# Kernel optimization log

Hardware: AMD Instinct MI355X
Metric: run time of the kernel (lower is better)

## Reference

```python
import jax, jax.numpy as jnp
import numpy as np

# Config matching init_kwargs: layer_nb=1 -> stride 16, image 608x608 -> 38x38 grid
B, CIN, H, W = 32, 512, 38, 38
NA, NC = 3, 80
STRIDE = 16.0
ANCHORS = np.array([[30.0, 61.0], [62.0, 45.0], [59.0, 119.0]], dtype=np.float32)


def setup_inputs() -> dict:
    key = jax.random.key(0)
    k1, k2, k3 = jax.random.split(key, 3)
    xin = jax.random.normal(k1, (B, CIN, H, W), dtype=jnp.float32)
    # 1x1 conv weight stored as (out_ch, in_ch); out_ch = NA*(NC+5) = 255
    conv_w = jax.random.normal(k2, (NA * (NC + 5), CIN), dtype=jnp.float32) * 0.02
    conv_b = jax.random.normal(k3, (NA * (NC + 5),), dtype=jnp.float32) * 0.01
    return {"xin": xin, "conv_w": conv_w, "conv_b": conv_b}


def reference(xin, conv_w, conv_b):
    # 1x1 conv == channel GEMM; fuse the NCHW->NHWC permute into the einsum
    fm = jnp.einsum('bchw,oc->bhwo', xin, conv_w) + conv_b  # [B,H,W,255]
    fm = fm.reshape(B, H, W, NA, NC + 5)
    tx, ty, tw, th = fm[..., 0], fm[..., 1], fm[..., 2], fm[..., 3]
    # grid offsets (precomputed via broadcasting instead of per-call numpy rebuild)
    x_off = jnp.arange(W, dtype=fm.dtype)[None, None, :, None]   # broadcast over B,H,NA
    y_off = jnp.arange(H, dtype=fm.dtype)[None, :, None, None]   # broadcast over B,W,NA
    anchors = jnp.asarray(ANCHORS, dtype=fm.dtype)               # [NA,2]
    bx = (jax.nn.sigmoid(tx) + x_off) * STRIDE
    by = (jax.nn.sigmoid(ty) + y_off) * STRIDE
    bw = jnp.exp(tw) * anchors[:, 0]
    bh = jnp.exp(th) * anchors[:, 1]
    boxes = jnp.stack([bx, by, bw, bh], axis=-1)                 # [B,H,W,NA,4]
    # concat decoded boxes with raw objectness + class logits -> [B,H,W,NA,85]
    return jnp.concatenate([boxes, fm[..., 4:]], axis=-1)
```

## Files before the change

kernel.cpp:

```cpp
#include <hip/hip_runtime.h>
#include <cstdint>
#include <cstddef>

#define CIN_K  512
#define WW_    38
#define BHW    1444
#define NOUT   255
#define MTOT   46208

#define BM 64
#define BK 32
#define KITERS (CIN_K / BK)
#define LDB 40
#define EPS_ 272

typedef __attribute__((ext_vector_type(8))) short  bf16x8;
typedef __attribute__((ext_vector_type(4))) float  floatx4;

static __device__ __forceinline__ unsigned f2bf(float f) {
    unsigned u = __builtin_bit_cast(unsigned, f);
    return (u + 0x7FFFu + ((u >> 16) & 1u)) >> 16;
}

__global__ void conv_w_to_bf16(const float* __restrict__ cw,
                               unsigned short* __restrict__ wb) {
    int tg   = blockIdx.x * 256 + threadIdx.x;
    int base = tg * 8;
    int n    = base >> 9;
    unsigned rr[4] = {0u, 0u, 0u, 0u};
    if (n < NOUT) {
        float4 v0 = *(const float4*)(cw + base);
        float4 v1 = *(const float4*)(cw + base + 4);
        rr[0] = f2bf(v0.x) | (f2bf(v0.y) << 16);
        rr[1] = f2bf(v0.z) | (f2bf(v0.w) << 16);
        rr[2] = f2bf(v1.x) | (f2bf(v1.y) << 16);
        rr[3] = f2bf(v1.z) | (f2bf(v1.w) << 16);
    }
    *(uint4*)(wb + base) = *(uint4*)rr;
}

__global__ __launch_bounds__(256, 3)
void yolo_head(const float* __restrict__ xin,
               const unsigned short* __restrict__ wb,
               const float* __restrict__ cb,
               float* __restrict__ out)
{
    __shared__ unsigned short Bs[256 * LDB];
    __shared__ float          EP[4 * 4 * EPS_];

    const int t    = threadIdx.x;
    const int w    = t >> 6;
    const int lane = t & 63;
    const int l15  = lane & 15;
    const int q    = lane >> 4;
    const int m0   = blockIdx.x * BM;

    const int m  = m0 + w * 16 + l15;
    const int bb = m / BHW;
    const int hw = m - bb * BHW;
    const float* pa = xin + (size_t)bb * (CIN_K * BHW) + hw + (size_t)(q * 8) * BHW;

    const int n0 = t >> 2;
    const int c4 = t & 3;
    const unsigned short* pb = wb + n0 * CIN_K + c4 * 8;

    floatx4 acc[16];
#pragma unroll
    for (int j = 0; j < 16; ++j) acc[j] = (floatx4){0.f, 0.f, 0.f, 0.f};

    float fa[8];
#pragma unroll
    for (int u = 0; u < 8; ++u) fa[u] = pa[(size_t)u * BHW];
    uint4 fbq[4];
#pragma unroll
    for (int s = 0; s < 4; ++s) fbq[s] = *(const uint4*)(pb + s * 64 * CIN_K);

#pragma unroll 1
    for (int it = 0; it < KITERS; ++it) {
        const int kn = (it < KITERS - 1 ? it + 1 : it) * BK;

        __syncthreads();
#pragma unroll
        for (int s = 0; s < 4; ++s)
            *(uint4*)(&Bs[(n0 + s * 64) * LDB + c4 * 8]) = fbq[s];
#pragma unroll
        for (int s = 0; s < 4; ++s)
            fbq[s] = *(const uint4*)(pb + kn + s * 64 * CIN_K);

        __syncthreads();

        unsigned pk[4];
#pragma unroll
        for (int u = 0; u < 4; ++u)
            pk[u] = f2bf(fa[2 * u]) | (f2bf(fa[2 * u + 1]) << 16);
        bf16x8 af = __builtin_bit_cast(bf16x8, *(int4*)pk);
#pragma unroll
        for (int u = 0; u < 8; ++u) fa[u] = pa[(size_t)(kn + u) * BHW];

#pragma unroll
        for (int j = 0; j < 16; ++j) {
            int4 v = *(const int4*)(&Bs[(j * 16 + l15) * LDB + q * 8]);
            acc[j] = __builtin_amdgcn_mfma_f32_16x16x32_bf16(
                         af, __builtin_bit_cast(bf16x8, v), acc[j], 0, 0, 0);
        }
    }

    float fw4[4], fh4[4];
#pragma unroll
    for (int r = 0; r < 4; ++r) {
        int mr  = m0 + w * 16 + q * 4 + r;
        int rem = mr % BHW;
        int hh  = rem / WW_;
        fh4[r] = (float)hh;
        fw4[r] = (float)(rem - hh * WW_);
    }

#pragma unroll
    for (int j = 0; j < 16; ++j) {
        int   n    = j * 16 + l15;
        int   nc   = n < NOUT ? n : NOUT - 1;
        int   ai   = nc / 85;
        int   ji   = nc - ai * 85;
        float bias = cb[nc];
#pragma unroll
        for (int r = 0; r < 4; ++r) {
            float v = acc[j][r] + bias;
            float res;
            if (ji == 0)      res = (1.f / (1.f + __expf(-v)) + fw4[r]) * 16.f;
            else if (ji == 1) res = (1.f / (1.f + __expf(-v)) + fh4[r]) * 16.f;
            else if (ji == 2) res = __expf(v) * ((ai == 0) ? 30.f : (ai == 1) ? 62.f : 59.f);
            else if (ji == 3) res = __expf(v) * ((ai == 0) ? 61.f : (ai == 1) ? 45.f : 119.f);
            else              res = v;
            acc[j][r] = res;
        }
    }

    float* EPw = EP + w * (4 * EPS_);
#pragma unroll 1
    for (int qp = 0; qp < 4; ++qp) {
        if (q == qp) {
#pragma unroll
            for (int j = 0; j < 16; ++j)
#pragma unroll
                for (int r = 0; r < 4; ++r)
                    EPw[r * EPS_ + j * 16 + l15] = acc[j][r];
        }
        float* outc = out + (size_t)(m0 + w * 16 + qp * 4) * NOUT;
#pragma unroll
        for (int s = 0; s < 4; ++s) {
            int i2 = lane + 64 * s;
            if (i2 < 255) {
                float vv[4];
#pragma unroll
                for (int e = 0; e < 4; ++e) {
                    int f   = 4 * i2 + e;
                    int mr2 = f / NOUT;
                    int x   = f - mr2 * NOUT;
                    vv[e]   = EPw[mr2 * EPS_ + x];
                }
                *(float4*)(outc + 4 * i2) = make_float4(vv[0], vv[1], vv[2], vv[3]);
            }
        }
    }
}

extern "C" void kernel_launch(void* const* d_in, const int* in_sizes, int n_in,
                              void* d_out, int out_size, void* d_ws, size_t ws_size,
                              hipStream_t stream) {
    const float* xin = (const float*)d_in[0];
    const float* cw  = (const float*)d_in[1];
    const float* cb  = (const float*)d_in[2];
    float*       out = (float*)d_out;
    unsigned short* wb = (unsigned short*)d_ws;

    hipLaunchKernelGGL(conv_w_to_bf16, dim3(64), dim3(256), 0, stream, cw, wb);
    hipLaunchKernelGGL(yolo_head, dim3(MTOT / BM), dim3(256), 0, stream,
                       xin, wb, cb, out);
}
```

Baseline: 218.0 us.

## Stage full bf16 A tile in LDS and read weights directly from global

The GEMM is restructured. Each block first loads its whole 64x512 activation tile, converts it to bf16 and stores it in LDS once. Each wave then owns a 64-column slice of the output and streams its weight fragments straight from global/L2, which removes the per-K-step LDS staging of B and the two barriers per iteration. The epilogue writes the whole 64x255 tile through the shared LDS buffer. The larger LDS footprint lowers occupancy to 2 blocks per SM, and the weights are now reread from cache by every wave.

```diff
diff --git a/kernel.cpp b/kernel.cpp
--- a/kernel.cpp
+++ b/kernel.cpp
@@ -8,11 +8,8 @@
 #define NOUT   255
 #define MTOT   46208
 
-#define BM 64
-#define BK 32
-#define KITERS (CIN_K / BK)
-#define LDB 40
-#define EPS_ 272
+#define ROW_E  520
+#define ROW_DW 260
 
 typedef __attribute__((ext_vector_type(8))) short  bf16x8;
 typedef __attribute__((ext_vector_type(4))) float  floatx4;
@@ -39,126 +36,130 @@
     *(uint4*)(wb + base) = *(uint4*)rr;
 }
 
-__global__ __launch_bounds__(256, 3)
+__global__ __launch_bounds__(256, 2)
 void yolo_head(const float* __restrict__ xin,
                const unsigned short* __restrict__ wb,
                const float* __restrict__ cb,
                float* __restrict__ out)
 {
-    __shared__ unsigned short Bs[256 * LDB];
-    __shared__ float          EP[4 * 4 * EPS_];
+    __shared__ unsigned int smem[64 * ROW_DW];
+    unsigned short* As = (unsigned short*)smem;
 
     const int t    = threadIdx.x;
     const int w    = t >> 6;
     const int lane = t & 63;
     const int l15  = lane & 15;
     const int q    = lane >> 4;
-    const int m0   = blockIdx.x * BM;
+    const int m0   = blockIdx.x * 64;
 
-    const int m  = m0 + w * 16 + l15;
-    const int bb = m / BHW;
-    const int hw = m - bb * BHW;
-    const float* pa = xin + (size_t)bb * (CIN_K * BHW) + hw + (size_t)(q * 8) * BHW;
+    {
+        const int mloc = lane;
+        int m  = m0 + mloc;
+        int bi = m / BHW;
+        int hw = m - bi * BHW;
+        const float* pa = xin + (size_t)bi * (CIN_K * BHW) + hw;
+#pragma unroll
+        for (int s = 0; s < 16; ++s) {
+            const int k0 = s * 32 + w * 8;
+            float v[8];
+#pragma unroll
+            for (int u = 0; u < 8; ++u) v[u] = pa[(size_t)(k0 + u) * BHW];
+            unsigned pk[4];
+#pragma unroll
+            for (int u2 = 0; u2 < 4; ++u2)
+                pk[u2] = f2bf(v[2 * u2]) | (f2bf(v[2 * u2 + 1]) << 16);
+            *(uint4*)(&As[mloc * ROW_E + k0]) = *(uint4*)pk;
+        }
+    }
+    __syncthreads();
 
-    const int n0 = t >> 2;
-    const int c4 = t & 3;
-    const unsigned short* pb = wb + n0 * CIN_K + c4 * 8;
+    floatx4 acc[4][4];
+#pragma unroll
+    for (int i = 0; i < 4; ++i)
+#pragma unroll
+        for (int j = 0; j < 4; ++j)
+            acc[i][j] = (floatx4){0.f, 0.f, 0.f, 0.f};
 
-    floatx4 acc[16];
-#pragma unroll
-    for (int j = 0; j < 16; ++j) acc[j] = (floatx4){0.f, 0.f, 0.f, 0.f};
-
-    float fa[8];
-#pragma unroll
-    for (int u = 0; u < 8; ++u) fa[u] = pa[(size_t)u * BHW];
-    uint4 fbq[4];
-#pragma unroll
-    for (int s = 0; s < 4; ++s) fbq[s] = *(const uint4*)(pb + s * 64 * CIN_K);
-
-#pragma unroll 1
-    for (int it = 0; it < KITERS; ++it) {
-        const int kn = (it < KITERS - 1 ? it + 1 : it) * BK;
-
-        __syncthreads();
-#pragma unroll
-        for (int s = 0; s < 4; ++s)
-            *(uint4*)(&Bs[(n0 + s * 64) * LDB + c4 * 8]) = fbq[s];
-#pragma unroll
-        for (int s = 0; s < 4; ++s)
-            fbq[s] = *(const uint4*)(pb + kn + s * 64 * CIN_K);
-
-        __syncthreads();
-
-        unsigned pk[4];
-#pragma unroll
-        for (int u = 0; u < 4; ++u)
-            pk[u] = f2bf(fa[2 * u]) | (f2bf(fa[2 * u + 1]) << 16);
-        bf16x8 af = __builtin_bit_cast(bf16x8, *(int4*)pk);
-#pragma unroll
-        for (int u = 0; u < 8; ++u) fa[u] = pa[(size_t)(kn + u) * BHW];
+    const unsigned short* pbw = wb + (size_t)(w * 64 + l15) * CIN_K + q * 8;
 
 #pragma unroll
-        for (int j = 0; j < 16; ++j) {
-            int4 v = *(const int4*)(&Bs[(j * 16 + l15) * LDB + q * 8]);
-            acc[j] = __builtin_amdgcn_mfma_f32_16x16x32_bf16(
-                         af, __builtin_bit_cast(bf16x8, v), acc[j], 0, 0, 0);
+    for (int kc = 0; kc < 16; ++kc) {
+        bf16x8 bfr[4], af[4];
+#pragma unroll
+        for (int j = 0; j < 4; ++j) {
+            uint4 bv = *(const uint4*)(pbw + (size_t)j * 16 * CIN_K + kc * 32);
+            bfr[j] = __builtin_bit_cast(bf16x8, bv);
         }
-    }
-
-    float fw4[4], fh4[4];
 #pragma unroll
-    for (int r = 0; r < 4; ++r) {
-        int mr  = m0 + w * 16 + q * 4 + r;
-        int rem = mr % BHW;
-        int hh  = rem / WW_;
-        fh4[r] = (float)hh;
-        fw4[r] = (float)(rem - hh * WW_);
+        for (int i = 0; i < 4; ++i) {
+            int4 av = *(const int4*)(&As[(i * 16 + l15) * ROW_E + kc * 32 + q * 8]);
+            af[i] = __builtin_bit_cast(bf16x8, av);
+        }
+#pragma unroll
+        for (int i = 0; i < 4; ++i)
+#pragma unroll
+            for (int j = 0; j < 4; ++j)
+                acc[i][j] = __builtin_amdgcn_mfma_f32_16x16x32_bf16(
+                                af[i], bfr[j], acc[i][j], 0, 0, 0);
     }
 
 #pragma unroll
-    for (int j = 0; j < 16; ++j) {
-        int   n    = j * 16 + l15;
+    for (int j = 0; j < 4; ++j) {
+        int   n    = w * 64 + j * 16 + l15;
         int   nc   = n < NOUT ? n : NOUT - 1;
         int   ai   = nc / 85;
         int   ji   = nc - ai * 85;
         float bias = cb[nc];
+        float aw   = (ai == 0) ? 30.f : (ai == 1) ? 62.f : 59.f;
+        float ah   = (ai == 0) ? 61.f : (ai == 1) ? 45.f : 119.f;
 #pragma unroll
-        for (int r = 0; r < 4; ++r) {
-            float v = acc[j][r] + bias;
-            float res;
-            if (ji == 0)      res = (1.f / (1.f + __expf(-v)) + fw4[r]) * 16.f;
-            else if (ji == 1) res = (1.f / (1.f + __expf(-v)) + fh4[r]) * 16.f;
-            else if (ji == 2) res = __expf(v) * ((ai == 0) ? 30.f : (ai == 1) ? 62.f : 59.f);
-            else if (ji == 3) res = __expf(v) * ((ai == 0) ? 61.f : (ai == 1) ? 45.f : 119.f);
-            else              res = v;
-            acc[j][r] = res;
-        }
+        for (int i = 0; i < 4; ++i)
+#pragma unroll
+            for (int r = 0; r < 4; ++r) {
+                int   md  = m0 + i * 16 + q * 4 + r;
+                int   rem = md % BHW;
+                int   hh  = rem / WW_;
+                float v   = acc[i][j][r] + bias;
+                float res;
+                if (ji == 0)      res = (1.f / (1.f + __expf(-v)) + (float)(rem - hh * WW_)) * 16.f;
+                else if (ji == 1) res = (1.f / (1.f + __expf(-v)) + (float)hh) * 16.f;
+                else if (ji == 2) res = __expf(v) * aw;
+                else if (ji == 3) res = __expf(v) * ah;
+                else              res = v;
+                acc[i][j][r] = res;
+            }
     }
 
-    float* EPw = EP + w * (4 * EPS_);
-#pragma unroll 1
-    for (int qp = 0; qp < 4; ++qp) {
-        if (q == qp) {
+    __syncthreads();
+    float* EP = (float*)smem;
+
 #pragma unroll
-            for (int j = 0; j < 16; ++j)
+    for (int i = 0; i < 4; ++i)
 #pragma unroll
-                for (int r = 0; r < 4; ++r)
-                    EPw[r * EPS_ + j * 16 + l15] = acc[j][r];
-        }
-        float* outc = out + (size_t)(m0 + w * 16 + qp * 4) * NOUT;
+        for (int j = 0; j < 4; ++j)
 #pragma unroll
-        for (int s = 0; s < 4; ++s) {
-            int i2 = lane + 64 * s;
-            if (i2 < 255) {
+            for (int r = 0; r < 4; ++r)
+                EP[(i * 16 + q * 4 + r) * ROW_DW + w * 64 + j * 16 + l15] = acc[i][j][r];
+
+    __syncthreads();
+
+    {
+        float*       ob  = out + (size_t)(m0 + w * 16) * NOUT;
+        const float* EPb = (const float*)smem + (w * 16) * ROW_DW;
+#pragma unroll
+        for (int s2 = 0; s2 < 16; ++s2) {
+            int f4 = s2 * 64 + lane;
+            if (f4 < 1020) {
+                int   f = f4 * 4;
                 float vv[4];
 #pragma unroll
                 for (int e = 0; e < 4; ++e) {
-                    int f   = 4 * i2 + e;
-                    int mr2 = f / NOUT;
-                    int x   = f - mr2 * NOUT;
-                    vv[e]   = EPw[mr2 * EPS_ + x];
+                    int fe = f + e;
+                    int mr = fe / NOUT;
+                    int x  = fe - mr * NOUT;
+                    vv[e]  = EPb[mr * ROW_DW + x];
                 }
-                *(float4*)(outc + 4 * i2) = make_float4(vv[0], vv[1], vv[2], vv[3]);
+                *(float4*)(ob + f) = make_float4(vv[0], vv[1], vv[2], vv[3]);
             }
         }
     }
@@ -174,6 +175,6 @@
     unsigned short* wb = (unsigned short*)d_ws;
 
     hipLaunchKernelGGL(conv_w_to_bf16, dim3(64), dim3(256), 0, stream, cw, wb);
-    hipLaunchKernelGGL(yolo_head, dim3(MTOT / BM), dim3(256), 0, stream,
+    hipLaunchKernelGGL(yolo_head, dim3(MTOT / 64), dim3(256), 0, stream,
                        xin, wb, cb, out);
 }
```

Measured after the change: 195.0 us. 1.12x faster.
